# Kernel tuning notes

Hardware: AMD Instinct MI355X
Metric: run time of the kernel (lower is better)

Reference implementation:

```python
import jax, jax.numpy as jnp
import numpy as np

N, H, INTER, M = 8192, 2048, 8192, 2
UP_OUT = 2 * INTER  # gated: up_gate produces interleaved (glu, linear) pairs
EPS = 1e-6
ALPHA = 1.702
LIMIT = 7.0


def setup_inputs() -> dict:
    key = jax.random.key(0)
    k1, k2, k3, k4 = jax.random.split(key, 4)
    x = jax.random.normal(k1, (N, H), dtype=jnp.float32)
    # token stream is pre-permuted so same-modality tokens are contiguous;
    # balanced groups: first N//2 tokens modality 0, rest modality 1
    modality_mapping = jnp.repeat(jnp.arange(M, dtype=jnp.int64), N // M)
    w_norm = jax.random.normal(k2, (H * M,), dtype=jnp.float32) * 0.02
    w_up = jax.random.normal(k3, (UP_OUT * M, H), dtype=jnp.float32) * 0.02
    w_down = jax.random.normal(k4, (H * M, INTER), dtype=jnp.float32) * 0.02
    return {"x": x, "modality_mapping": modality_mapping,
            "w_norm": w_norm, "w_up": w_up, "w_down": w_down}


def reference(x, modality_mapping, w_norm, w_up, w_down):
    # x: [N, H], pre-grouped into M equal contiguous modality chunks.
    n, h = x.shape
    g = n // M  # tokens per modality group
    # ---- MultiModalityRMSNorm (effective weight = 1 + w) ----
    t = x * jax.lax.rsqrt(jnp.mean(x * x, axis=-1, keepdims=True) + EPS)
    tm = t.reshape(M, g, h)                       # [M, g, H]
    tm = tm * (w_norm.reshape(M, 1, h) + 1.0)
    # ---- PackedExpertLinear up_gate: per-modality weight chunk ----
    Wu = w_up.reshape(M, UP_OUT, h)               # [M, 2*INTER, H]
    y = jnp.einsum('mgh,moh->mgo', tm, Wu)        # [M, g, 2*INTER]
    # ---- swiglu7: clamped gated SwiGLU with +1 linear bias ----
    y_glu = jnp.minimum(y[..., ::2], LIMIT)
    y_lin = jnp.clip(y[..., 1::2], -LIMIT, LIMIT)
    a = y_glu * jax.nn.sigmoid(ALPHA * y_glu) * (y_lin + 1.0)  # [M, g, INTER]
    # ---- PackedExpertLinear down_proj ----
    Wd = w_down.reshape(M, h, INTER)              # [M, H, INTER]
    z = jnp.einsum('mgi,mhi->mgh', a, Wd)         # [M, g, H]
    return z.reshape(n, h)
```

## Files before the change

### kernel.cpp

```cpp
#include <hip/hip_runtime.h>
#include <hip/hip_bf16.h>

#define DEVI __device__ __forceinline__

typedef __bf16 bf16x8 __attribute__((ext_vector_type(8)));
typedef float f32x4 __attribute__((ext_vector_type(4)));

namespace {

constexpr int H = 2048;
constexpr int INTER = 8192;
constexpr int M_MOD = 2;
constexpr int N_TOK = 8192;
constexpr int G = N_TOK / M_MOD;
constexpr int UP_OUT = 2 * INTER;

DEVI unsigned short f2bf(float f) {
  unsigned u = __builtin_bit_cast(unsigned, f);
  u += 0x7fffu + ((u >> 16) & 1u);
  return (unsigned short)(u >> 16);
}

DEVI void gload_lds16(const void* g, void* lds) {
  __builtin_amdgcn_global_load_lds(
      (const __attribute__((address_space(1))) unsigned int*)g,
      (__attribute__((address_space(3))) unsigned int*)lds, 16, 0, 0);
}

DEVI void memfence_barrier() {
  asm volatile("" ::: "memory");
  __builtin_amdgcn_s_barrier();
  asm volatile("" ::: "memory");
}

__global__ __launch_bounds__(256) void cvt_f32_bf16(
    const float* __restrict__ in, unsigned short* __restrict__ out, int n4) {
  int idx = blockIdx.x * blockDim.x + threadIdx.x;
  int stride = gridDim.x * blockDim.x;
  for (int i = idx; i < n4; i += stride) {
    float4 v = ((const float4*)in)[i];
    ushort4 o;
    o.x = f2bf(v.x); o.y = f2bf(v.y); o.z = f2bf(v.z); o.w = f2bf(v.w);
    ((ushort4*)out)[i] = o;
  }
}

__global__ __launch_bounds__(256) void rmsnorm_kernel(
    const float* __restrict__ x, const float* __restrict__ w_norm,
    unsigned short* __restrict__ tm) {
  const int row = blockIdx.x;
  const int mod = row >> 12;
  const int t = threadIdx.x;
  const float4* xr = (const float4*)(x + (size_t)row * H);
  const float4* wr = (const float4*)(w_norm + (size_t)mod * H);

  float4 v0 = xr[t];
  float4 v1 = xr[t + 256];
  float ss = v0.x * v0.x + v0.y * v0.y + v0.z * v0.z + v0.w * v0.w +
             v1.x * v1.x + v1.y * v1.y + v1.z * v1.z + v1.w * v1.w;
  #pragma unroll
  for (int o = 32; o > 0; o >>= 1) ss += __shfl_down(ss, o);
  __shared__ float red[4];
  const int w = t >> 6, l = t & 63;
  if (l == 0) red[w] = ss;
  __syncthreads();
  float tot = red[0] + red[1] + red[2] + red[3];
  float rn = rsqrtf(tot * (1.0f / H) + 1e-6f);

  float4 w0 = wr[t];
  float4 w1 = wr[t + 256];
  ushort4 o0, o1;
  o0.x = f2bf(v0.x * rn * (1.f + w0.x));
  o0.y = f2bf(v0.y * rn * (1.f + w0.y));
  o0.z = f2bf(v0.z * rn * (1.f + w0.z));
  o0.w = f2bf(v0.w * rn * (1.f + w0.w));
  o1.x = f2bf(v1.x * rn * (1.f + w1.x));
  o1.y = f2bf(v1.y * rn * (1.f + w1.y));
  o1.z = f2bf(v1.z * rn * (1.f + w1.z));
  o1.w = f2bf(v1.w * rn * (1.f + w1.w));
  ushort4* tr = (ushort4*)(tm + (size_t)row * H);
  tr[t] = o0;
  tr[t + 256] = o1;
}

template <int K, int CT_PER_MOD, int EPI>
__global__ __launch_bounds__(512, 2) void gemm8p(
    const unsigned short* __restrict__ A0, const unsigned short* __restrict__ B0,
    void* __restrict__ O0, long sAm, long sBm, long sOm) {
  __shared__ __align__(16) char smem[2][2][32768];

  constexpr int NT = K / 64;
  constexpr int HMAX = 4 * NT;
  constexpr int NITER = NT / 2;
  constexpr int PER_MOD = 16 * CT_PER_MOD;
  constexpr int NWG = 2 * PER_MOD;
  constexpr int CPX = NWG / 8;

  const int bid0 = blockIdx.x;
  const int bid = (bid0 % 8) * CPX + bid0 / 8;
  const int mod = bid / PER_MOD;
  const int q = bid % PER_MOD;
  const int ct = q / 16;
  const int rt = q % 16;

  const unsigned short* A = A0 + (long)mod * sAm;
  const unsigned short* B = B0 + (long)mod * sBm;

  const int t = threadIdx.x;
  const int w = t >> 6;
  const int l = t & 63;
  const int wr = w >> 2;
  const int wc = w & 3;

  const int fr = l & 15;
  const int fk = l >> 4;
  const int frx = (fr & 7) << 4;

  const unsigned short* gArow = A + (size_t)rt * 256 * K;
  const unsigned short* gBrow = B + (size_t)ct * 256 * K;
  const int srow = t >> 3;
  const int scol = ((t & 7) ^ (srow & 7)) * 8;

  auto stage = [&](int h) {
    if (h >= HMAX) h -= HMAX;
    const int tt = h >> 2, qq = h & 3;
    const int isB = qq >> 1, half = qq & 1, buf = tt & 1;
    const unsigned short* src = (isB ? gBrow : gArow) +
        (size_t)(half * 128 + srow) * K + tt * 64 + scol;
    char* dst = smem[buf][isB] + half * 16384 + t * 16;
    gload_lds16(src, dst);
    gload_lds16(src + (size_t)64 * K, dst + 8192);
  };

  auto rdA = [&](const char* base, int mi, int ks) -> bf16x8 {
    const int row = wr * 128 + mi * 16 + fr;
    return *(const bf16x8*)(base + row * 128 + ((((ks << 2) + fk) << 4) ^ frx));
  };
  auto rdB = [&](const char* base, int ni, int ks) -> bf16x8 {
    const int row = wc * 64 + ni * 16 + fr;
    return *(const bf16x8*)(base + row * 128 + ((((ks << 2) + fk) << 4) ^ frx));
  };

  f32x4 acc[8][4];
  #pragma unroll
  for (int m = 0; m < 8; ++m)
    #pragma unroll
    for (int n = 0; n < 4; ++n) acc[m][n] = (f32x4){0.f, 0.f, 0.f, 0.f};

  bf16x8 aF[4], aF2[4], bF[4], bF2[4];

#define RDA4(DST, BASE, MLO, KS)                                              \
  _Pragma("unroll") for (int mi = 0; mi < 4; ++mi)                            \
      DST[mi] = rdA(BASE, (MLO) + mi, KS);
#define RDB4(DST, BASE, KS)                                                   \
  _Pragma("unroll") for (int ni = 0; ni < 4; ++ni) DST[ni] = rdB(BASE, ni, KS);
#define MFMAQ(AR, BR, MLO)                                                    \
  __builtin_amdgcn_s_setprio(1);                                              \
  _Pragma("unroll") for (int mi = 0; mi < 4; ++mi)                            \
  _Pragma("unroll") for (int ni = 0; ni < 4; ++ni)                            \
    acc[(MLO) + mi][ni] = __builtin_amdgcn_mfma_f32_16x16x32_bf16(            \
        AR[mi], BR[ni], acc[(MLO) + mi][ni], 0, 0, 0);                        \
  __builtin_amdgcn_s_setprio(0);

  stage(0); stage(1); stage(2); stage(3);
  asm volatile("s_waitcnt vmcnt(0)" ::: "memory");
  memfence_barrier();

  const char* A0b = smem[0][0];
  const char* B0b = smem[0][1];
  const char* A1b = smem[1][0];
  const char* B1b = smem[1][1];

  for (int i = 0; i < NITER; ++i) {
    const int h0 = 8 * i;
    RDA4(aF, A0b, 0, 0);
    RDB4(bF, B0b, 0);
    stage(h0 + 4); stage(h0 + 6); stage(h0 + 7);
    RDA4(aF2, A0b, 4, 0);
    MFMAQ(aF, bF, 0);
    stage(h0 + 5);
    RDA4(aF, A0b, 0, 1);
    RDB4(bF2, B0b, 1);
    MFMAQ(aF2, bF, 4);
    RDA4(aF2, A0b, 4, 1);
    MFMAQ(aF, bF2, 0);
    MFMAQ(aF2, bF2, 4);
    asm volatile("s_waitcnt vmcnt(0)" ::: "memory");
    memfence_barrier();

    RDA4(aF, A1b, 0, 0);
    RDB4(bF, B1b, 0);
    stage(h0 + 8); stage(h0 + 10); stage(h0 + 11);
    RDA4(aF2, A1b, 4, 0);
    MFMAQ(aF, bF, 0);
    stage(h0 + 9);
    RDA4(aF, A1b, 0, 1);
    RDB4(bF2, B1b, 1);
    MFMAQ(aF2, bF, 4);
    RDA4(aF2, A1b, 4, 1);
    MFMAQ(aF, bF2, 0);
    MFMAQ(aF2, bF2, 4);
    asm volatile("s_waitcnt vmcnt(0)" ::: "memory");
    memfence_barrier();
  }
#undef MFMAQ
#undef RDA4
#undef RDB4

  const int row0 = rt * 256 + wr * 128 + (l >> 4) * 4;
  const int col0 = ct * 256 + wc * 64 + (l & 15);
  if (EPI == 0) {
    unsigned short* Oa = (unsigned short*)O0 + (long)mod * sOm;
    #pragma unroll
    for (int m = 0; m < 8; ++m)
      #pragma unroll
      for (int n = 0; n < 4; ++n)
        #pragma unroll
        for (int j = 0; j < 4; ++j) {
          float y = acc[m][n][j];
          float p = __shfl_xor(y, 1);
          if (!(l & 1)) {
            float glu = fminf(y, 7.f);
            float lin = fminf(fmaxf(p, -7.f), 7.f);
            float sg = 1.f / (1.f + __expf(-1.702f * glu));
            float av = glu * sg * (lin + 1.f);
            Oa[(size_t)(row0 + m * 16 + j) * INTER + ((col0 + n * 16) >> 1)] = f2bf(av);
          }
        }
  } else {
    float* Oz = (float*)O0 + (long)mod * sOm;
    #pragma unroll
    for (int m = 0; m < 8; ++m)
      #pragma unroll
      for (int n = 0; n < 4; ++n)
        #pragma unroll
        for (int j = 0; j < 4; ++j)
          Oz[(size_t)(row0 + m * 16 + j) * H + (col0 + n * 16)] = acc[m][n][j];
  }
}

}

extern "C" void kernel_launch(void* const* d_in, const int* in_sizes, int n_in,
                              void* d_out, int out_size, void* d_ws, size_t ws_size,
                              hipStream_t stream) {
  const float* x = (const float*)d_in[0];
  const float* w_norm = (const float*)d_in[2];
  const float* w_up = (const float*)d_in[3];
  const float* w_down = (const float*)d_in[4];

  char* ws = (char*)d_ws;
  unsigned short* wup_bf = (unsigned short*)ws;
  unsigned short* wdn_bf = (unsigned short*)(ws + 134217728L);
  unsigned short* tm = (unsigned short*)(ws + 201326592L);
  unsigned short* abuf = (unsigned short*)(ws + 234881024L);

  cvt_f32_bf16<<<2048, 256, 0, stream>>>(w_up, wup_bf, (UP_OUT * M_MOD * H) / 4);
  cvt_f32_bf16<<<2048, 256, 0, stream>>>(w_down, wdn_bf, (H * M_MOD * INTER) / 4);
  rmsnorm_kernel<<<N_TOK, 256, 0, stream>>>(x, w_norm, tm);

  gemm8p<H, UP_OUT / 256, 0>
      <<<M_MOD * 16 * (UP_OUT / 256), 512, 0, stream>>>(
          tm, wup_bf, abuf, (long)G * H, (long)UP_OUT * H, (long)G * INTER);

  gemm8p<INTER, H / 256, 1>
      <<<M_MOD * 16 * (H / 256), 512, 0, stream>>>(
          abuf, wdn_bf, d_out, (long)G * INTER, (long)H * INTER, (long)G * H);
}
```

Baseline: 849.5 us.

## Load B operand directly from global into registers, bypassing LDS

The GEMM stops staging the B (weight) tile through shared memory. Each wave now loads its B fragments straight from global memory into registers, prefetching one k-slice ahead, while only A stays double-buffered in LDS. This halves the LDS footprint and removes the LDS writes and reads for B. In exchange, the two wave-rows each fetch the same B data, the global access pattern is row-strided with little coalescing, and load latency may be exposed at the vmcnt(0) waits. The last prefetch also reads past the end of K.

```diff
diff --git a/kernel.cpp b/kernel.cpp
--- a/kernel.cpp
+++ b/kernel.cpp
@@ -87,10 +87,9 @@
 __global__ __launch_bounds__(512, 2) void gemm8p(
     const unsigned short* __restrict__ A0, const unsigned short* __restrict__ B0,
     void* __restrict__ O0, long sAm, long sBm, long sOm) {
-  __shared__ __align__(16) char smem[2][2][32768];
+  __shared__ __align__(16) char smem[2][32768];
 
   constexpr int NT = K / 64;
-  constexpr int HMAX = 4 * NT;
   constexpr int NITER = NT / 2;
   constexpr int PER_MOD = 16 * CT_PER_MOD;
   constexpr int NWG = 2 * PER_MOD;
@@ -117,17 +116,14 @@
   const int frx = (fr & 7) << 4;
 
   const unsigned short* gArow = A + (size_t)rt * 256 * K;
-  const unsigned short* gBrow = B + (size_t)ct * 256 * K;
   const int srow = t >> 3;
   const int scol = ((t & 7) ^ (srow & 7)) * 8;
 
-  auto stage = [&](int h) {
-    if (h >= HMAX) h -= HMAX;
-    const int tt = h >> 2, qq = h & 3;
-    const int isB = qq >> 1, half = qq & 1, buf = tt & 1;
-    const unsigned short* src = (isB ? gBrow : gArow) +
-        (size_t)(half * 128 + srow) * K + tt * 64 + scol;
-    char* dst = smem[buf][isB] + half * 16384 + t * 16;
+  auto stageA = [&](int tt_, int half) {
+    if (tt_ >= NT) tt_ -= NT;
+    const unsigned short* src = gArow + (size_t)(half * 128 + srow) * K +
+                                tt_ * 64 + scol;
+    char* dst = smem[tt_ & 1] + half * 16384 + t * 16;
     gload_lds16(src, dst);
     gload_lds16(src + (size_t)64 * K, dst + 8192);
   };
@@ -136,10 +132,18 @@
     const int row = wr * 128 + mi * 16 + fr;
     return *(const bf16x8*)(base + row * 128 + ((((ks << 2) + fk) << 4) ^ frx));
   };
-  auto rdB = [&](const char* base, int ni, int ks) -> bf16x8 {
-    const int row = wc * 64 + ni * 16 + fr;
-    return *(const bf16x8*)(base + row * 128 + ((((ks << 2) + fk) << 4) ^ frx));
-  };
+
+  const char* Bb = (const char*)(B + (size_t)ct * 256 * K);
+  unsigned boff0 = (unsigned)(((size_t)(wc * 64 + 0 * 16 + fr) * K + fk * 8) * 2);
+  unsigned boff1 = (unsigned)(((size_t)(wc * 64 + 1 * 16 + fr) * K + fk * 8) * 2);
+  unsigned boff2 = (unsigned)(((size_t)(wc * 64 + 2 * 16 + fr) * K + fk * 8) * 2);
+  unsigned boff3 = (unsigned)(((size_t)(wc * 64 + 3 * 16 + fr) * K + fk * 8) * 2);
+
+#define LDB4(DST, OFF)                                                        \
+  DST[0] = *(const bf16x8*)(Bb + boff0 + (OFF));                              \
+  DST[1] = *(const bf16x8*)(Bb + boff1 + (OFF));                              \
+  DST[2] = *(const bf16x8*)(Bb + boff2 + (OFF));                              \
+  DST[3] = *(const bf16x8*)(Bb + boff3 + (OFF));
 
   f32x4 acc[8][4];
   #pragma unroll
@@ -152,8 +156,6 @@
 #define RDA4(DST, BASE, MLO, KS)                                              \
   _Pragma("unroll") for (int mi = 0; mi < 4; ++mi)                            \
       DST[mi] = rdA(BASE, (MLO) + mi, KS);
-#define RDB4(DST, BASE, KS)                                                   \
-  _Pragma("unroll") for (int ni = 0; ni < 4; ++ni) DST[ni] = rdB(BASE, ni, KS);
 #define MFMAQ(AR, BR, MLO)                                                    \
   __builtin_amdgcn_s_setprio(1);                                              \
   _Pragma("unroll") for (int mi = 0; mi < 4; ++mi)                            \
@@ -162,42 +164,42 @@
         AR[mi], BR[ni], acc[(MLO) + mi][ni], 0, 0, 0);                        \
   __builtin_amdgcn_s_setprio(0);
 
-  stage(0); stage(1); stage(2); stage(3);
+  stageA(0, 0); stageA(0, 1);
+  LDB4(bF, 0);
   asm volatile("s_waitcnt vmcnt(0)" ::: "memory");
   memfence_barrier();
 
-  const char* A0b = smem[0][0];
-  const char* B0b = smem[0][1];
-  const char* A1b = smem[1][0];
-  const char* B1b = smem[1][1];
+  const char* A0b = smem[0];
+  const char* A1b = smem[1];
 
   for (int i = 0; i < NITER; ++i) {
-    const int h0 = 8 * i;
     RDA4(aF, A0b, 0, 0);
-    RDB4(bF, B0b, 0);
-    stage(h0 + 4); stage(h0 + 6); stage(h0 + 7);
+    LDB4(bF2, 64);
+    stageA(2 * i + 1, 0);
     RDA4(aF2, A0b, 4, 0);
     MFMAQ(aF, bF, 0);
-    stage(h0 + 5);
+    stageA(2 * i + 1, 1);
     RDA4(aF, A0b, 0, 1);
-    RDB4(bF2, B0b, 1);
     MFMAQ(aF2, bF, 4);
     RDA4(aF2, A0b, 4, 1);
+    LDB4(bF, 128);
+    boff0 += 128; boff1 += 128; boff2 += 128; boff3 += 128;
     MFMAQ(aF, bF2, 0);
     MFMAQ(aF2, bF2, 4);
     asm volatile("s_waitcnt vmcnt(0)" ::: "memory");
     memfence_barrier();
 
     RDA4(aF, A1b, 0, 0);
-    RDB4(bF, B1b, 0);
-    stage(h0 + 8); stage(h0 + 10); stage(h0 + 11);
+    LDB4(bF2, 64);
+    stageA(2 * i + 2, 0);
     RDA4(aF2, A1b, 4, 0);
     MFMAQ(aF, bF, 0);
-    stage(h0 + 9);
+    stageA(2 * i + 2, 1);
     RDA4(aF, A1b, 0, 1);
-    RDB4(bF2, B1b, 1);
     MFMAQ(aF2, bF, 4);
     RDA4(aF2, A1b, 4, 1);
+    LDB4(bF, 128);
+    boff0 += 128; boff1 += 128; boff2 += 128; boff3 += 128;
     MFMAQ(aF, bF2, 0);
     MFMAQ(aF2, bF2, 4);
     asm volatile("s_waitcnt vmcnt(0)" ::: "memory");
@@ -205,7 +207,7 @@
   }
 #undef MFMAQ
 #undef RDA4
-#undef RDB4
+#undef LDB4
 
   const int row0 = rt * 256 + wr * 128 + (l >> 4) * 4;
   const int col0 = ct * 256 + wc * 64 + (l & 15);
```

Measured after the change: 1.167 ms. +37.4%, slower.
